# Kernel optimization log

Hardware: AMD Instinct MI355X
Metric: run time of the kernel (lower is better)

The kernel has to match this reference:

```python
import jax, jax.numpy as jnp
import numpy as np

N_EMBED = 2048
N_HEAD = 16
HEAD_SIZE = N_EMBED // N_HEAD  # 128


def rotate_half(x):
    x1, x2 = jnp.split(x, 2, axis=-1)
    return jnp.concatenate((-x2, x1), axis=-1)


def setup_inputs() -> dict:
    key = jax.random.key(0)
    k_x, k_qkv, k_proj, k_b = jax.random.split(key, 4)
    B, T = 4, 2048
    x = jax.random.normal(k_x, (B, T, N_EMBED), dtype=jnp.float32)
    # weights stored as [in, out] so y = x @ W (equivalent param'n of nn.Linear)
    w_qkv = jax.random.normal(k_qkv, (N_EMBED, 3 * N_EMBED), dtype=jnp.float32) * (N_EMBED ** -0.5)
    w_proj = jax.random.normal(k_proj, (N_EMBED, N_EMBED), dtype=jnp.float32) * (N_EMBED ** -0.5)
    b_proj = jax.random.normal(k_b, (N_EMBED,), dtype=jnp.float32) * 0.02
    return {"x": x, "w_qkv": w_qkv, "w_proj": w_proj, "b_proj": b_proj}


def reference(x, w_qkv, w_proj, b_proj):
    B, T, C = x.shape
    H, D = N_HEAD, HEAD_SIZE
    qkv = x @ w_qkv                                   # [B,T,3C]
    q, k, v = jnp.split(qkv, 3, axis=2)
    q = q.reshape(B, T, H, D).transpose(0, 2, 1, 3)   # [B,H,T,D]
    k = k.reshape(B, T, H, D).transpose(0, 2, 1, 3)
    v = v.reshape(B, T, H, D).transpose(0, 2, 1, 3)
    # RoPE in fp32
    inv_freq = 1.0 / (10000.0 ** (jnp.arange(0, D, 2, dtype=jnp.float32) / D))
    t = jnp.arange(T, dtype=jnp.float32)
    freqs = jnp.einsum('i,j->ij', t, inv_freq)        # [T,D/2]
    emb = jnp.concatenate((freqs, freqs), axis=-1)    # [T,D]
    cos = jnp.cos(emb)[None, None, :, :]
    sin = jnp.sin(emb)[None, None, :, :]
    qf = q.astype(jnp.float32)
    kf = k.astype(jnp.float32)
    q = (qf * cos + rotate_half(qf) * sin).astype(v.dtype)
    k = (kf * cos + rotate_half(kf) * sin).astype(v.dtype)
    # causal SDPA
    scale = 1.0 / jnp.sqrt(jnp.asarray(D, dtype=q.dtype))
    scores = jnp.einsum('bhqd,bhkd->bhqk', q, k) * scale
    causal = jnp.tril(jnp.ones((T, T), dtype=bool))
    scores = jnp.where(causal[None, None, :, :], scores, jnp.finfo(scores.dtype).min)
    attn = jax.nn.softmax(scores, axis=-1)
    out = jnp.einsum('bhqk,bhkd->bhqd', attn, v)      # [B,H,T,D]
    out = out.transpose(0, 2, 1, 3).reshape(B, T, C)
    return out @ w_proj + b_proj
```

## Files before the change

### kernel.cpp

```cpp
#include <hip/hip_runtime.h>
#include <hip/hip_bf16.h>
#include <cstdint>
#include <cstddef>

typedef __bf16 bf16x8 __attribute__((ext_vector_type(8)));
typedef __bf16 bf16x4 __attribute__((ext_vector_type(4)));
typedef float  f32x4  __attribute__((ext_vector_type(4)));

__device__ __forceinline__ void lds_load16(const void* gsrc, void* ldst) {
    __builtin_amdgcn_global_load_lds(
        (const __attribute__((address_space(1))) unsigned int*)gsrc,
        (__attribute__((address_space(3))) unsigned int*)ldst,
        16, 0, 0);
}

__global__ __launch_bounds__(256) void cvt_k(const float* __restrict__ in,
                                             __bf16* __restrict__ out, int n8) {
    int i = blockIdx.x * 256 + threadIdx.x;
    if (i >= n8) return;
    const float4* p4 = (const float4*)in + (size_t)i * 2;
    float4 a = p4[0], b = p4[1];
    bf16x8 o;
    o[0] = (__bf16)a.x; o[1] = (__bf16)a.y; o[2] = (__bf16)a.z; o[3] = (__bf16)a.w;
    o[4] = (__bf16)b.x; o[5] = (__bf16)b.y; o[6] = (__bf16)b.z; o[7] = (__bf16)b.w;
    *((bf16x8*)out + i) = o;
}

__global__ __launch_bounds__(256) void transp_k(const float* __restrict__ W,
                                                __bf16* __restrict__ WT, int R, int C) {
    __shared__ float tile[32][33];
    int tx = threadIdx.x & 31, ty = threadIdx.x >> 5;
    int c0 = blockIdx.x * 32, r0 = blockIdx.y * 32;
#pragma unroll
    for (int k = 0; k < 4; ++k)
        tile[ty + 8 * k][tx] = W[(size_t)(r0 + ty + 8 * k) * C + c0 + tx];
    __syncthreads();
#pragma unroll
    for (int k = 0; k < 4; ++k)
        WT[(size_t)(c0 + ty + 8 * k) * R + r0 + tx] = (__bf16)tile[tx][ty + 8 * k];
}

__global__ __launch_bounds__(256) void sincos_k(float2* __restrict__ sc) {
    int idx = blockIdx.x * 256 + threadIdx.x;
    int t = idx >> 6, j = idx & 63;
    float inv = powf(10000.f, -(float)j / 64.f);
    float f = (float)t * inv;
    float s, c;
    sincosf(f, &s, &c);
    sc[idx] = make_float2(c, s);
}

__global__ __launch_bounds__(512, 2) void gemm8_k(const __bf16* __restrict__ A,
                                                  const __bf16* __restrict__ Bt,
                                                  int nbn, int mode,
                                                  __bf16* __restrict__ qb, __bf16* __restrict__ kb,
                                                  __bf16* __restrict__ vt,
                                                  float* __restrict__ outp,
                                                  const float* __restrict__ bias,
                                                  const float2* __restrict__ sc) {
    __shared__ __bf16 lds[2][2][2][128 * 64];
    const int K = 2048, NT = K / 64;
    int nwg = gridDim.x;
    int per = nwg >> 3;
    int bid = blockIdx.x;
    int wg = (bid & 7) * per + (bid >> 3);
    int bm = wg / nbn, bn = wg % nbn;
    int m0 = bm * 256, n0 = bn * 256;
    int tid = threadIdx.x;
    int lane = tid & 63, wave = tid >> 6;
    int wm = wave >> 2, wn = wave & 3;
    int lr = lane & 15, lg = lane >> 4;

    f32x4 acc[8][4] = {};

    auto stageA = [&](int db, int sub, int kt) {
#pragma unroll
        for (int l = 0; l < 2; ++l) {
            int chunk = l * 512 + tid;
            int r = chunk >> 3, c16 = chunk & 7;
            int rg = m0 + ((r >> 6) << 7) + (sub << 6) + (r & 63);
            lds_load16(A + (size_t)rg * K + (kt << 6) + ((c16 ^ (r & 7)) << 3),
                       &lds[db][0][sub][chunk * 8]);
        }
    };
    auto stageB = [&](int db, int sub, int kt) {
#pragma unroll
        for (int l = 0; l < 2; ++l) {
            int chunk = l * 512 + tid;
            int r = chunk >> 3, c16 = chunk & 7;
            int rg = n0 + ((r >> 5) << 6) + (sub << 5) + (r & 31);
            lds_load16(Bt + (size_t)rg * K + (kt << 6) + ((c16 ^ (r & 7)) << 3),
                       &lds[db][1][sub][chunk * 8]);
        }
    };
    auto rdA = [&](int db, int sub, int q, int kk) -> bf16x8 {
        int r = (wm << 6) + (q << 4) + lr;
        int cb = ((kk << 6) + (lg << 4)) ^ ((r & 7) << 4);
        return *(const bf16x8*)((const char*)&lds[db][0][sub][0] + r * 128 + cb);
    };
    auto rdB = [&](int db, int j, int kk) -> bf16x8 {
        int sub = j >> 1;
        int r = (wn << 5) + ((j & 1) << 4) + lr;
        int cb = ((kk << 6) + (lg << 4)) ^ ((r & 7) << 4);
        return *(const bf16x8*)((const char*)&lds[db][1][sub][0] + r * 128 + cb);
    };

    stageA(0, 0, 0); stageB(0, 0, 0); stageB(0, 1, 0); stageA(0, 1, 0);
    asm volatile("s_waitcnt vmcnt(4)" ::: "memory");
    __builtin_amdgcn_s_barrier();

    bf16x8 a[4][2], bA[2][2], bB[2][2];
    for (int t = 0; t < NT; ++t) {
        int db = t & 1, dn = db ^ 1;
        bool pf = (t + 1 < NT);
#pragma unroll
        for (int q = 0; q < 4; ++q) { a[q][0] = rdA(db, 0, q, 0); a[q][1] = rdA(db, 0, q, 1); }
#pragma unroll
        for (int j = 0; j < 2; ++j) { bA[j][0] = rdB(db, j, 0); bA[j][1] = rdB(db, j, 1); }
        if (pf) stageA(dn, 0, t + 1);
        __builtin_amdgcn_s_barrier();
        asm volatile("s_waitcnt lgkmcnt(0)" ::: "memory");
        __builtin_amdgcn_sched_barrier(0);
        __builtin_amdgcn_s_setprio(1);
#pragma unroll
        for (int q = 0; q < 4; ++q)
#pragma unroll
            for (int j = 0; j < 2; ++j)
#pragma unroll
                for (int kk = 0; kk < 2; ++kk)
                    acc[q][j] = __builtin_amdgcn_mfma_f32_16x16x32_bf16(a[q][kk], bA[j][kk], acc[q][j], 0, 0, 0);
        __builtin_amdgcn_s_setprio(0);
        if (pf) asm volatile("s_waitcnt vmcnt(4)" ::: "memory");
        else    asm volatile("s_waitcnt vmcnt(2)" ::: "memory");
        __builtin_amdgcn_s_barrier();
#pragma unroll
        for (int j = 0; j < 2; ++j) { bB[j][0] = rdB(db, j + 2, 0); bB[j][1] = rdB(db, j + 2, 1); }
        if (pf) stageB(dn, 0, t + 1);
        __builtin_amdgcn_s_barrier();
        asm volatile("s_waitcnt lgkmcnt(0)" ::: "memory");
        __builtin_amdgcn_sched_barrier(0);
        __builtin_amdgcn_s_setprio(1);
#pragma unroll
        for (int q = 0; q < 4; ++q)
#pragma unroll
            for (int j = 0; j < 2; ++j)
#pragma unroll
                for (int kk = 0; kk < 2; ++kk)
                    acc[q][j + 2] = __builtin_amdgcn_mfma_f32_16x16x32_bf16(a[q][kk], bB[j][kk], acc[q][j + 2], 0, 0, 0);
        __builtin_amdgcn_s_setprio(0);
        if (pf) asm volatile("s_waitcnt vmcnt(4)" ::: "memory");
        else    asm volatile("s_waitcnt vmcnt(0)" ::: "memory");
        __builtin_amdgcn_s_barrier();
#pragma unroll
        for (int q = 0; q < 4; ++q) { a[q][0] = rdA(db, 1, q, 0); a[q][1] = rdA(db, 1, q, 1); }
        if (pf) stageB(dn, 1, t + 1);
        __builtin_amdgcn_s_barrier();
        asm volatile("s_waitcnt lgkmcnt(0)" ::: "memory");
        __builtin_amdgcn_sched_barrier(0);
        __builtin_amdgcn_s_setprio(1);
#pragma unroll
        for (int q = 0; q < 4; ++q)
#pragma unroll
            for (int j = 0; j < 2; ++j)
#pragma unroll
                for (int kk = 0; kk < 2; ++kk)
                    acc[q + 4][j + 2] = __builtin_amdgcn_mfma_f32_16x16x32_bf16(a[q][kk], bB[j][kk], acc[q + 4][j + 2], 0, 0, 0);
        __builtin_amdgcn_s_setprio(0);
        __builtin_amdgcn_s_barrier();
        if (pf) stageA(dn, 1, t + 1);
        __builtin_amdgcn_s_setprio(1);
#pragma unroll
        for (int q = 0; q < 4; ++q)
#pragma unroll
            for (int j = 0; j < 2; ++j)
#pragma unroll
                for (int kk = 0; kk < 2; ++kk)
                    acc[q + 4][j] = __builtin_amdgcn_mfma_f32_16x16x32_bf16(a[q][kk], bA[j][kk], acc[q + 4][j], 0, 0, 0);
        __builtin_amdgcn_s_setprio(0);
        if (pf) asm volatile("s_waitcnt vmcnt(4)" ::: "memory");
        __builtin_amdgcn_s_barrier();
    }

    if (mode == 0) {
        int which = n0 >> 11;
        if (which == 2) {
#pragma unroll
            for (int q = 0; q < 8; ++q) {
                int row_t = (wm << 7) + ((q >> 2) << 6) + ((q & 3) << 4) + (lg << 2);
#pragma unroll
                for (int j = 0; j < 4; ++j) {
                    int c = n0 + (wn << 6) + (j << 4) + lr;
                    int h = (c & 2047) >> 7, d = c & 127;
#pragma unroll
                    for (int r = 0; r < 4; ++r) {
                        int row = m0 + row_t + r;
                        int b_ = row >> 11, tt = row & 2047;
                        vt[((size_t)(b_ * 16 + h) * 128 + d) * 2048 + tt] = (__bf16)acc[q][j][r];
                    }
                }
            }
        } else {
            __bf16* dst = (which == 0) ? qb : kb;
            float scale = (which == 0) ? 0.08838834764831845f : 1.f;
            int rl = (wm << 4) + (lg << 2);
            int colw = (wn << 6);
#pragma unroll
            for (int q = 0; q < 8; ++q) {
                float* scr = (float*)&lds[q & 1][0][0][0];
                int row_t = (wm << 7) + ((q >> 2) << 6) + ((q & 3) << 4) + (lg << 2);
#pragma unroll
                for (int j = 0; j < 4; ++j)
#pragma unroll
                    for (int r = 0; r < 4; ++r)
                        scr[(rl + r) * 260 + colw + (j << 4) + lr] = acc[q][j][r];
                __syncthreads();
#pragma unroll
                for (int j = 0; j < 4; ++j) {
                    int c = n0 + colw + (j << 4) + lr;
                    int h = (c & 2047) >> 7, d = c & 127;
                    int jj = (j << 4) + lr;
#pragma unroll
                    for (int r = 0; r < 4; ++r) {
                        int row = m0 + row_t + r;
                        int b_ = row >> 11, tt = row & 2047;
                        float2 cs = sc[tt * 64 + jj];
                        float v0 = acc[q][j][r];
                        float v1 = scr[(rl + r) * 260 + (colw ^ 64) + (j << 4) + lr];
                        float o = ((wn & 1) == 0) ? (v0 * cs.x - v1 * cs.y)
                                                  : (v0 * cs.x + v1 * cs.y);
                        dst[((size_t)(b_ * 16 + h) * 2048 + tt) * 128 + d] = (__bf16)(o * scale);
                    }
                }
            }
        }
    } else {
#pragma unroll
        for (int q = 0; q < 8; ++q) {
            int row_t = (wm << 7) + ((q >> 2) << 6) + ((q & 3) << 4) + (lg << 2);
#pragma unroll
            for (int j = 0; j < 4; ++j) {
                int col = n0 + (wn << 6) + (j << 4) + lr;
                float bv = bias[col];
#pragma unroll
                for (int r = 0; r < 4; ++r) {
                    int row = m0 + row_t + r;
                    outp[(size_t)row * 2048 + col] = acc[q][j][r] + bv;
                }
            }
        }
    }
}

__global__ __launch_bounds__(512, 2) void attn_k(const __bf16* __restrict__ qb,
                                                 const __bf16* __restrict__ kb,
                                                 const __bf16* __restrict__ vt,
                                                 __bf16* __restrict__ ao) {
    __shared__ __bf16 Ks[64 * 128];
    __shared__ __bf16 Vs[128 * 64];
    __shared__ __bf16 Ps[8][16 * 64];

    int bid = blockIdx.x;
    int qt = 15 - (bid >> 6);
    int bh = bid & 63;
    int qs = qt * 128;
    int tid = threadIdx.x, wave = tid >> 6, lane = tid & 63;
    int lr = lane & 15, lg = lane >> 4;

    bf16x8 qf[4];
    const __bf16* Qrow = qb + ((size_t)bh * 2048 + qs + wave * 16 + lr) * 128;
#pragma unroll
    for (int kk = 0; kk < 4; ++kk) qf[kk] = *(const bf16x8*)(Qrow + kk * 32 + lg * 8);

    f32x4 ot[8] = {};
    float m_run = -1e30f, l_run = 0.f;
    int qmax = qs + wave * 16 + 15;
    int kend = qs + 64;

    for (int ks = 0; ks <= kend; ks += 64) {
#pragma unroll
        for (int i = 0; i < 2; ++i) {
            int c = tid + i * 512;
            {
                int row = c >> 4;
                int cc = c ^ (row & 7);
                int dd = (cc & 15) * 8;
                lds_load16(kb + ((size_t)bh * 2048 + ks + row) * 128 + dd, Ks + c * 8);
            }
            {
                int row = c >> 3;
                int cc = c ^ (row & 7);
                int tt = (cc & 7) * 8;
                lds_load16(vt + ((size_t)bh * 128 + row) * 2048 + ks + tt, Vs + c * 8);
            }
        }
        __syncthreads();

        if (ks <= qmax) {
            f32x4 st[4];
            __builtin_amdgcn_s_setprio(1);
#pragma unroll
            for (int mt = 0; mt < 4; ++mt) {
                f32x4 s = {};
#pragma unroll
                for (int kk = 0; kk < 4; ++kk) {
                    int row = mt * 16 + lr;
                    const __bf16* kp = Ks + row * 128 + ((((kk * 64 + lg * 16)) ^ ((row & 7) << 4)) >> 1);
                    bf16x8 afr = *(const bf16x8*)kp;
                    s = __builtin_amdgcn_mfma_f32_16x16x32_bf16(afr, qf[kk], s, 0, 0, 0);
                }
                st[mt] = s;
            }
            __builtin_amdgcn_s_setprio(0);

            if (ks + 63 > qs + wave * 16) {
                int q = qs + wave * 16 + lr;
#pragma unroll
                for (int mt = 0; mt < 4; ++mt)
#pragma unroll
                    for (int r = 0; r < 4; ++r) {
                        int kv = ks + mt * 16 + lg * 4 + r;
                        if (kv > q) st[mt][r] = -1e30f;
                    }
            }

            float pm = -1e30f;
#pragma unroll
            for (int mt = 0; mt < 4; ++mt)
#pragma unroll
                for (int r = 0; r < 4; ++r) pm = fmaxf(pm, st[mt][r]);
            pm = fmaxf(pm, __shfl_xor(pm, 16));
            pm = fmaxf(pm, __shfl_xor(pm, 32));
            float nm = fmaxf(m_run, pm);
            float alpha = __expf(m_run - nm);
            float psum = 0.f;
#pragma unroll
            for (int mt = 0; mt < 4; ++mt)
#pragma unroll
                for (int r = 0; r < 4; ++r) {
                    float p = __expf(st[mt][r] - nm);
                    psum += p;
                    st[mt][r] = p;
                }
            psum += __shfl_xor(psum, 16);
            psum += __shfl_xor(psum, 32);
            l_run = l_run * alpha + psum;
            m_run = nm;
#pragma unroll
            for (int t8 = 0; t8 < 8; ++t8) ot[t8] *= alpha;

#pragma unroll
            for (int mt = 0; mt < 4; ++mt) {
                bf16x4 pk;
#pragma unroll
                for (int r = 0; r < 4; ++r) pk[r] = (__bf16)st[mt][r];
                int byteoff = lr * 128 + (((mt * 32 + lg * 8)) ^ ((lr & 7) << 4));
                *(bf16x4*)((char*)&Ps[wave][0] + byteoff) = pk;
            }

            bf16x8 pfr[2];
#pragma unroll
            for (int kk = 0; kk < 2; ++kk) {
                const char* pp = (const char*)&Ps[wave][0] + lr * 128 + (((kk * 64 + lg * 16)) ^ ((lr & 7) << 4));
                pfr[kk] = *(const bf16x8*)pp;
            }
            __builtin_amdgcn_s_setprio(1);
#pragma unroll
            for (int dt = 0; dt < 8; ++dt) {
#pragma unroll
                for (int kk = 0; kk < 2; ++kk) {
                    int row = dt * 16 + lr;
                    const __bf16* vp = Vs + row * 64 + ((((kk * 64 + lg * 16)) ^ ((row & 7) << 4)) >> 1);
                    bf16x8 afr = *(const bf16x8*)vp;
                    ot[dt] = __builtin_amdgcn_mfma_f32_16x16x32_bf16(afr, pfr[kk], ot[dt], 0, 0, 0);
                }
            }
            __builtin_amdgcn_s_setprio(0);
        }
        __syncthreads();
    }

    float inv = 1.f / l_run;
    int b_ = bh >> 4, h = bh & 15;
    size_t rowbase = ((size_t)b_ * 2048 + qs + wave * 16 + lr) * 2048 + h * 128;
#pragma unroll
    for (int dt = 0; dt < 8; ++dt) {
        bf16x4 o;
#pragma unroll
        for (int r = 0; r < 4; ++r) o[r] = (__bf16)(ot[dt][r] * inv);
        *(bf16x4*)(ao + rowbase + dt * 16 + lg * 4) = o;
    }
}

extern "C" void kernel_launch(void* const* d_in, const int* in_sizes, int n_in,
                              void* d_out, int out_size, void* d_ws, size_t ws_size,
                              hipStream_t stream) {
    const float* x      = (const float*)d_in[0];
    const float* w_qkv  = (const float*)d_in[1];
    const float* w_proj = (const float*)d_in[2];
    const float* b_proj = (const float*)d_in[3];
    float* out = (float*)d_out;
    char* ws = (char*)d_ws;

    __bf16* xb  = (__bf16*)(ws);
    __bf16* wqt = (__bf16*)(ws + 33554432);
    __bf16* wpt = (__bf16*)(ws + 58720256);
    __bf16* qb  = (__bf16*)(ws + 67108864);
    __bf16* kb  = (__bf16*)(ws + 100663296);
    __bf16* vt  = (__bf16*)(ws + 134217728);
    __bf16* ao  = (__bf16*)(ws + 167772160);
    float2* sc  = (float2*)(ws + 201326592);

    hipLaunchKernelGGL(cvt_k, dim3(8192), dim3(256), 0, stream, x, xb, 2097152);
    hipLaunchKernelGGL(transp_k, dim3(192, 64), dim3(256), 0, stream, w_qkv, wqt, 2048, 6144);
    hipLaunchKernelGGL(transp_k, dim3(64, 64), dim3(256), 0, stream, w_proj, wpt, 2048, 2048);
    hipLaunchKernelGGL(sincos_k, dim3(512), dim3(256), 0, stream, sc);
    hipLaunchKernelGGL(gemm8_k, dim3(768), dim3(512), 0, stream,
                       xb, wqt, 24, 0, qb, kb, vt, (float*)nullptr, (const float*)nullptr, sc);
    hipLaunchKernelGGL(attn_k, dim3(1024), dim3(512), 0, stream, qb, kb, vt, ao);
    hipLaunchKernelGGL(gemm8_k, dim3(256), dim3(512), 0, stream,
                       ao, wpt, 8, 1, (__bf16*)nullptr, (__bf16*)nullptr, (__bf16*)nullptr,
                       out, b_proj, (const float2*)nullptr);
}
```

Measured before the change: 394.2 us.

## Double-buffer K/V tiles in attention kernel with async LDS prefetch

```diff
diff --git a/kernel.cpp b/kernel.cpp
--- a/kernel.cpp
+++ b/kernel.cpp
@@ -255,8 +255,8 @@
                                                  const __bf16* __restrict__ kb,
                                                  const __bf16* __restrict__ vt,
                                                  __bf16* __restrict__ ao) {
-    __shared__ __bf16 Ks[64 * 128];
-    __shared__ __bf16 Vs[128 * 64];
+    __shared__ __bf16 Ks[2][64 * 128];
+    __shared__ __bf16 Vs[2][128 * 64];
     __shared__ __bf16 Ps[8][16 * 64];
 
     int bid = blockIdx.x;
@@ -274,9 +274,11 @@
     f32x4 ot[8] = {};
     float m_run = -1e30f, l_run = 0.f;
     int qmax = qs + wave * 16 + 15;
-    int kend = qs + 64;
-
-    for (int ks = 0; ks <= kend; ks += 64) {
+    int nt = (qs >> 6) + 2;
+
+    auto stage = [&](int it) {
+        int b = it & 1;
+        int ks = it << 6;
 #pragma unroll
         for (int i = 0; i < 2; ++i) {
             int c = tid + i * 512;
@@ -284,16 +286,28 @@
                 int row = c >> 4;
                 int cc = c ^ (row & 7);
                 int dd = (cc & 15) * 8;
-                lds_load16(kb + ((size_t)bh * 2048 + ks + row) * 128 + dd, Ks + c * 8);
+                lds_load16(kb + ((size_t)bh * 2048 + ks + row) * 128 + dd, &Ks[b][c * 8]);
             }
             {
                 int row = c >> 3;
                 int cc = c ^ (row & 7);
                 int tt = (cc & 7) * 8;
-                lds_load16(vt + ((size_t)bh * 128 + row) * 2048 + ks + tt, Vs + c * 8);
-            }
-        }
-        __syncthreads();
+                lds_load16(vt + ((size_t)bh * 128 + row) * 2048 + ks + tt, &Vs[b][c * 8]);
+            }
+        }
+    };
+
+    stage(0);
+    for (int it = 0; it < nt; ++it) {
+        int ks = it << 6;
+        int b = it & 1;
+        if (it + 1 < nt) {
+            stage(it + 1);
+            asm volatile("s_waitcnt vmcnt(4)" ::: "memory");
+        } else {
+            asm volatile("s_waitcnt vmcnt(0)" ::: "memory");
+        }
+        __builtin_amdgcn_s_barrier();
 
         if (ks <= qmax) {
             f32x4 st[4];
@@ -304,7 +318,7 @@
 #pragma unroll
                 for (int kk = 0; kk < 4; ++kk) {
                     int row = mt * 16 + lr;
-                    const __bf16* kp = Ks + row * 128 + ((((kk * 64 + lg * 16)) ^ ((row & 7) << 4)) >> 1);
+                    const __bf16* kp = &Ks[b][0] + row * 128 + ((((kk * 64 + lg * 16)) ^ ((row & 7) << 4)) >> 1);
                     bf16x8 afr = *(const bf16x8*)kp;
                     s = __builtin_amdgcn_mfma_f32_16x16x32_bf16(afr, qf[kk], s, 0, 0, 0);
                 }
@@ -369,14 +383,14 @@
 #pragma unroll
                 for (int kk = 0; kk < 2; ++kk) {
                     int row = dt * 16 + lr;
-                    const __bf16* vp = Vs + row * 64 + ((((kk * 64 + lg * 16)) ^ ((row & 7) << 4)) >> 1);
+                    const __bf16* vp = &Vs[b][0] + row * 64 + ((((kk * 64 + lg * 16)) ^ ((row & 7) << 4)) >> 1);
                     bf16x8 afr = *(const bf16x8*)vp;
                     ot[dt] = __builtin_amdgcn_mfma_f32_16x16x32_bf16(afr, pfr[kk], ot[dt], 0, 0, 0);
                 }
             }
             __builtin_amdgcn_s_setprio(0);
         }
-        __syncthreads();
+        __builtin_amdgcn_s_barrier();
     }
 
     float inv = 1.f / l_run;
```

Result: no change. 398.1 us (+1.0%).
